# Performance work log

Measured on AMD Instinct MI355X. Metric: run time of the kernel, lower is better.

## Reference

```python
import jax, jax.numpy as jnp
import numpy as np

D, DFF, H = 768, 3072, 12
HD = D // H
EPS = 1e-12

def _ln(t, gamma, beta):
    mu = t.mean(-1, keepdims=True)
    var = jnp.mean((t - mu) ** 2, -1, keepdims=True)
    return gamma * (t - mu) / jnp.sqrt(var + EPS) + beta

def setup_inputs() -> dict:
    key = jax.random.key(0)
    ks = jax.random.split(key, 16)
    s = 0.02
    x = jax.random.normal(ks[0], (2, 2048, D), jnp.float32)
    mask = jnp.ones((2, 2048), jnp.float32)
    def lin(k, out_d, in_d):
        kw, kb = jax.random.split(k)
        return (jax.random.normal(kw, (out_d, in_d), jnp.float32) * s,
                jnp.zeros((out_d,), jnp.float32))
    Wq, bq = lin(ks[1], D, D)
    Wk, bk = lin(ks[2], D, D)
    Wv, bv = lin(ks[3], D, D)
    Wp, bp = lin(ks[4], D, D)
    W1, bf1 = lin(ks[5], DFF, D)
    W2, bf2 = lin(ks[6], D, DFF)
    g1 = jnp.ones((D,), jnp.float32); be1 = jnp.zeros((D,), jnp.float32)
    g2 = jnp.ones((D,), jnp.float32); be2 = jnp.zeros((D,), jnp.float32)
    return dict(x=x, mask=mask, Wq=Wq, bq=bq, Wk=Wk, bk=bk, Wv=Wv, bv=bv,
                Wp=Wp, bp=bp, g1=g1, be1=be1, W1=W1, bf1=bf1, W2=W2, bf2=bf2,
                g2=g2, be2=be2)

def reference(x, mask, Wq, bq, Wk, bk, Wv, bv, Wp, bp, g1, be1, W1, bf1, W2, bf2, g2, be2):
    B, S, _ = x.shape
    # projections (torch Linear: x @ W^T + b)
    q = (x @ Wq.T + bq).reshape(B, S, H, HD).transpose(0, 2, 1, 3)  # [B,H,S,HD]
    k = (x @ Wk.T + bk).reshape(B, S, H, HD).transpose(0, 2, 1, 3)
    v = (x @ Wv.T + bv).reshape(B, S, H, HD).transpose(0, 2, 1, 3)
    scores = jnp.einsum('bhqd,bhkd->bhqk', q, k) / jnp.sqrt(jnp.float32(HD))
    scores = scores - 10000.0 * (1.0 - mask[:, None, None, :])
    p = jax.nn.softmax(scores, axis=-1)  # dropout is identity at eval
    h = jnp.einsum('bhqk,bhkd->bqhd', p, v).reshape(B, S, D)
    h = h @ Wp.T + bp
    x1 = _ln(x + h, g1, be1)
    ff = jax.nn.gelu(x1 @ W1.T + bf1, approximate=False) @ W2.T + bf2
    return _ln(x1 + ff, g2, be2)
```

## Files before the change

kernel.cpp:

```cpp
#include <hip/hip_runtime.h>
#include <hip/hip_bf16.h>
#include <math.h>

#define D_MODEL 768
#define D_FF    3072
#define N_HEAD  12
#define HEAD_D  64
#define BATCH   2
#define SEQ     2048
#define QKV_LD  2304

typedef __attribute__((ext_vector_type(8))) short short8;
typedef __attribute__((ext_vector_type(8))) unsigned short ushort8;
typedef __attribute__((ext_vector_type(4))) float f32x4;

__device__ inline unsigned short f2bf(float f) {
    union { __hip_bfloat16 b; unsigned short u; } cv;
    cv.b = __float2bfloat16(f);
    return cv.u;
}

__device__ inline float bf2f(unsigned short u) {
    union { unsigned int i; float f; } cv;
    cv.i = ((unsigned int)u) << 16;
    return cv.f;
}

__device__ inline void async_load16(const void* g, void* l) {
    __builtin_amdgcn_global_load_lds(
        (const __attribute__((address_space(1))) void*)g,
        (__attribute__((address_space(3))) void*)l, 16, 0, 0);
}

__global__ __launch_bounds__(256) void conv_fused(
    const float* __restrict__ x,
    const float* __restrict__ Wq, const float* __restrict__ Wk,
    const float* __restrict__ Wv, const float* __restrict__ Wp,
    const float* __restrict__ W1, const float* __restrict__ W2,
    const float* __restrict__ bq, const float* __restrict__ bk,
    const float* __restrict__ bv,
    unsigned short* __restrict__ xb, unsigned short* __restrict__ wqkvb,
    unsigned short* __restrict__ wpb, unsigned short* __restrict__ w1b,
    unsigned short* __restrict__ w2b, float* __restrict__ bqkv)
{
    int bid = blockIdx.x;
    const float* src; unsigned short* dst; int base;
    if      (bid < 3072) { src = x;  dst = xb;              base = bid;        }
    else if (bid < 3648) { src = Wq; dst = wqkvb;           base = bid - 3072; }
    else if (bid < 4224) { src = Wk; dst = wqkvb + 589824;  base = bid - 3648; }
    else if (bid < 4800) { src = Wv; dst = wqkvb + 1179648; base = bid - 4224; }
    else if (bid < 5376) { src = Wp; dst = wpb;             base = bid - 4800; }
    else if (bid < 7680) { src = W1; dst = w1b;             base = bid - 5376; }
    else if (bid < 9984) { src = W2; dst = w2b;             base = bid - 7680; }
    else {
        for (int j = threadIdx.x; j < QKV_LD; j += 256)
            bqkv[j] = (j < 768) ? bq[j] : (j < 1536) ? bk[j - 768] : bv[j - 1536];
        return;
    }
    int i = (base * 256 + threadIdx.x) * 4;
    float4 v = *(const float4*)(src + i);
    ushort4 o4;
    o4.x = f2bf(v.x); o4.y = f2bf(v.y); o4.z = f2bf(v.z); o4.w = f2bf(v.w);
    *(ushort4*)(dst + i) = o4;
}

#define NSTAGE 3

__global__ __launch_bounds__(256) void gemm_bf16(
    const unsigned short* __restrict__ A, int lda,
    const unsigned short* __restrict__ W, int ldw,
    const float* __restrict__ bias,
    const unsigned short* __restrict__ resb, int ldr,
    float* __restrict__ outf, unsigned short* __restrict__ outb,
    float* __restrict__ pacc, int ldo,
    int M, int N, int K, int mode)
{
    __shared__ unsigned short As[NSTAGE][128 * 32];
    __shared__ unsigned short Bs[NSTAGE][128 * 32];

    const int t    = threadIdx.x;
    const int lane = t & 63;
    const int wv   = t >> 6;
    const int wm   = wv >> 1;
    const int wn   = wv & 1;
    const int bm   = blockIdx.y * 128;
    const int bn   = blockIdx.x * 128;
    const int kz   = blockIdx.z;
    const int Kc   = K / gridDim.z;

    const int qd   = lane >> 4;
    const int l16  = lane & 15;

    f32x4 acc[4][4];
    #pragma unroll
    for (int i = 0; i < 4; i++)
        #pragma unroll
        for (int j = 0; j < 4; j++)
            acc[i][j] = (f32x4){0.f, 0.f, 0.f, 0.f};

    const int srow = lane >> 2;
    const int sseg = (lane & 3) * 8;
    const int r0   = (wv * 2 + 0) * 16 + srow;
    const int r1   = (wv * 2 + 1) * 16 + srow;
    const size_t gA0 = (size_t)(bm + r0) * lda + sseg;
    const size_t gA1 = (size_t)(bm + r1) * lda + sseg;
    const size_t gB0 = (size_t)(bn + r0) * ldw + sseg;
    const size_t gB1 = (size_t)(bn + r1) * ldw + sseg;
    const int c0 = (wv * 2 + 0) * 512;
    const int c1 = (wv * 2 + 1) * 512;

    const int kbeg  = kz * Kc;
    const int niter = Kc / 32;

    async_load16(A + gA0 + kbeg, &As[0][c0]);
    async_load16(W + gB0 + kbeg, &Bs[0][c0]);
    async_load16(A + gA1 + kbeg, &As[0][c1]);
    async_load16(W + gB1 + kbeg, &Bs[0][c1]);
    if (niter > 1) {
        async_load16(A + gA0 + kbeg + 32, &As[1][c0]);
        async_load16(W + gB0 + kbeg + 32, &Bs[1][c0]);
        async_load16(A + gA1 + kbeg + 32, &As[1][c1]);
        async_load16(W + gB1 + kbeg + 32, &Bs[1][c1]);
    }
    if (niter > 2) {
        async_load16(A + gA0 + kbeg + 64, &As[2][c0]);
        async_load16(W + gB0 + kbeg + 64, &Bs[2][c0]);
        async_load16(A + gA1 + kbeg + 64, &As[2][c1]);
        async_load16(W + gB1 + kbeg + 64, &Bs[2][c1]);
    }

    int stage = 0;
    for (int it = 0; it < niter; it++) {
        const int rem = niter - 1 - it;
        if (rem >= 2)      __builtin_amdgcn_s_waitcnt(0x0F78);
        else if (rem == 1) __builtin_amdgcn_s_waitcnt(0x0F74);
        else               __builtin_amdgcn_s_waitcnt(0x0F70);
        __builtin_amdgcn_s_barrier();

        short8 af[4], bf[4];
        #pragma unroll
        for (int mt = 0; mt < 4; mt++)
            af[mt] = *(const short8*)(&As[stage][(wm * 64 + mt * 16 + l16) * 32 + qd * 8]);
        #pragma unroll
        for (int nt = 0; nt < 4; nt++)
            bf[nt] = *(const short8*)(&Bs[stage][(wn * 64 + nt * 16 + l16) * 32 + qd * 8]);
        #pragma unroll
        for (int mt = 0; mt < 4; mt++)
            #pragma unroll
            for (int nt = 0; nt < 4; nt++)
                acc[mt][nt] = __builtin_amdgcn_mfma_f32_16x16x32_bf16(
                    af[mt], bf[nt], acc[mt][nt], 0, 0, 0);

        __builtin_amdgcn_s_barrier();
        if (it + NSTAGE < niter) {
            const int kn = kbeg + (it + NSTAGE) * 32;
            async_load16(A + gA0 + kn, &As[stage][c0]);
            async_load16(W + gB0 + kn, &Bs[stage][c0]);
            async_load16(A + gA1 + kn, &As[stage][c1]);
            async_load16(W + gB1 + kn, &Bs[stage][c1]);
        }
        stage = (stage == NSTAGE - 1) ? 0 : stage + 1;
    }

    #pragma unroll
    for (int mt = 0; mt < 4; mt++) {
        #pragma unroll
        for (int nt = 0; nt < 4; nt++) {
            int col = bn + wn * 64 + nt * 16 + l16;
            float bv = (kz == 0) ? bias[col] : 0.f;
            #pragma unroll
            for (int r = 0; r < 4; r++) {
                int row = bm + wm * 64 + mt * 16 + qd * 4 + r;
                if (kz != 0) {
                    pacc[(size_t)row * ldo + col] = acc[mt][nt][r];
                    continue;
                }
                float v = acc[mt][nt][r] + bv;
                if (mode == 1) {
                    v += bf2f(resb[(size_t)row * ldr + col]);
                    outf[(size_t)row * ldo + col] = v;
                } else if (mode == 2) {
                    v = 0.5f * v * (1.0f + erff(v * 0.70710678118654752f));
                    outb[(size_t)row * ldo + col] = f2bf(v);
                } else if (mode == 3) {
                    outb[(size_t)row * ldo + col] = f2bf(v);
                } else {
                    outf[(size_t)row * ldo + col] = v;
                }
            }
        }
    }
}

#define ASTR 72

__global__ __launch_bounds__(256) void attn_mfma(
    const unsigned short* __restrict__ qkv, const float* __restrict__ mask,
    unsigned short* __restrict__ out)
{
    __shared__ __align__(16) unsigned short Ks[64 * ASTR];
    __shared__ __align__(16) unsigned short Vt[64 * ASTR];
    __shared__ float Ms[64];

    const int t    = threadIdx.x;
    const int lane = t & 63;
    const int wv   = t >> 6;
    const int l16  = lane & 15;
    const int quad = lane >> 4;
    const int q0   = blockIdx.x * 64;
    const int bh   = blockIdx.y;
    const int h    = bh % N_HEAD;
    const int b    = bh / N_HEAD;

    const unsigned short* qb = qkv + (size_t)b * SEQ * QKV_LD + h * HEAD_D;
    const unsigned short* kb = qb + 768;
    const unsigned short* vb = qb + 1536;

    const int srow = t >> 2;
    const int sc0  = (t & 3) * 16;
    const int sigrow = (srow & 0x23) | ((srow & 0x04) << 2) | ((srow & 0x18) >> 1);
    const int vslot  = srow ^ ((t & 3) << 3);

    {
        const ushort8* src = (const ushort8*)(qb + (size_t)(q0 + srow) * QKV_LD + sc0);
        *(ushort8*)&Ks[srow * ASTR + sc0]     = src[0];
        *(ushort8*)&Ks[srow * ASTR + sc0 + 8] = src[1];
    }
    __syncthreads();
    short8 bq0 = *(const short8*)&Ks[(wv * 16 + l16) * ASTR + quad * 8];
    short8 bq1 = *(const short8*)&Ks[(wv * 16 + l16) * ASTR + 32 + quad * 8];
    __syncthreads();

    f32x4 o[4];
    #pragma unroll
    for (int i = 0; i < 4; i++) o[i] = (f32x4){0.f, 0.f, 0.f, 0.f};
    float m_st = -INFINITY, l_st = 0.f;

    for (int kt = 0; kt < SEQ / 64; kt++) {
        const int key0 = kt * 64;
        {
            const ushort8* ksrc = (const ushort8*)(kb + (size_t)(key0 + srow) * QKV_LD + sc0);
            *(ushort8*)&Ks[sigrow * ASTR + sc0]     = ksrc[0];
            *(ushort8*)&Ks[sigrow * ASTR + sc0 + 8] = ksrc[1];
            const ushort8* vsrc = (const ushort8*)(vb + (size_t)(key0 + srow) * QKV_LD + sc0);
            ushort8 v0 = vsrc[0], v1 = vsrc[1];
            #pragma unroll
            for (int j = 0; j < 8; j++) Vt[(sc0 + j) * ASTR + vslot] = v0[j];
            #pragma unroll
            for (int j = 0; j < 8; j++) Vt[(sc0 + 8 + j) * ASTR + vslot] = v1[j];
            if (t < 64) Ms[t] = -10000.0f * (1.0f - mask[b * SEQ + key0 + t]);
        }
        __syncthreads();

        f32x4 st[4];
        #pragma unroll
        for (int bi = 0; bi < 4; bi++) {
            const int krow = (bi * 16 + l16) * ASTR;
            short8 k0 = *(const short8*)&Ks[krow + quad * 8];
            short8 k1 = *(const short8*)&Ks[krow + 32 + quad * 8];
            f32x4 z = (f32x4){0.f, 0.f, 0.f, 0.f};
            z = __builtin_amdgcn_mfma_f32_16x16x32_bf16(k0, bq0, z, 0, 0, 0);
            st[bi] = __builtin_amdgcn_mfma_f32_16x16x32_bf16(k1, bq1, z, 0, 0, 0);
        }

        float p[4][4];
        float mx = -3.0e38f;
        #pragma unroll
        for (int bi = 0; bi < 4; bi++) {
            #pragma unroll
            for (int r = 0; r < 4; r++) {
                float s = fmaf(st[bi][r], 0.125f,
                               Ms[((bi >> 1) << 5) + (quad << 3) + ((bi & 1) << 2) + r]);
                p[bi][r] = s;
                mx = fmaxf(mx, s);
            }
        }
        mx = fmaxf(mx, __shfl_xor(mx, 16, 64));
        mx = fmaxf(mx, __shfl_xor(mx, 32, 64));
        float m_new = fmaxf(m_st, mx);
        float alpha = __expf(m_st - m_new);
        m_st = m_new;
        float ls = 0.f;
        #pragma unroll
        for (int bi = 0; bi < 4; bi++) {
            #pragma unroll
            for (int r = 0; r < 4; r++) {
                p[bi][r] = __expf(p[bi][r] - m_new);
                ls += p[bi][r];
            }
        }
        ls += __shfl_xor(ls, 16, 64);
        ls += __shfl_xor(ls, 32, 64);
        l_st = l_st * alpha + ls;

        float ar[4];
        #pragma unroll
        for (int r = 0; r < 4; r++) ar[r] = __shfl(alpha, quad * 4 + r, 64);
        #pragma unroll
        for (int nt = 0; nt < 4; nt++)
            #pragma unroll
            for (int r = 0; r < 4; r++)
                o[nt][r] *= ar[r];

        short8 pf0, pf1;
        #pragma unroll
        for (int bsel = 0; bsel < 2; bsel++) {
            #pragma unroll
            for (int r = 0; r < 4; r++) {
                pf0[bsel * 4 + r] = (short)f2bf(p[bsel][r]);
                pf1[bsel * 4 + r] = (short)f2bf(p[2 + bsel][r]);
            }
        }

        #pragma unroll
        for (int nt = 0; nt < 4; nt++) {
            const int vrow = (nt * 16 + l16) * ASTR;
            short8 v0 = *(const short8*)&Vt[vrow + ((quad * 8) ^ (nt << 3))];
            short8 v1 = *(const short8*)&Vt[vrow + ((32 + quad * 8) ^ (nt << 3))];
            o[nt] = __builtin_amdgcn_mfma_f32_16x16x32_bf16(pf0, v0, o[nt], 0, 0, 0);
            o[nt] = __builtin_amdgcn_mfma_f32_16x16x32_bf16(pf1, v1, o[nt], 0, 0, 0);
        }
        __syncthreads();
    }

    float inv = 1.0f / l_st;
    float ir[4];
    #pragma unroll
    for (int r = 0; r < 4; r++) ir[r] = __shfl(inv, quad * 4 + r, 64);
    #pragma unroll
    for (int nt = 0; nt < 4; nt++) {
        #pragma unroll
        for (int r = 0; r < 4; r++) {
            int qi = q0 + wv * 16 + quad * 4 + r;
            out[(size_t)(b * SEQ + qi) * D_MODEL + h * HEAD_D + nt * 16 + l16] =
                f2bf(o[nt][r] * ir[r]);
        }
    }
}

__global__ __launch_bounds__(256) void ln_kernel(
    const float* __restrict__ in, const float* __restrict__ in2,
    const float* __restrict__ g, const float* __restrict__ be,
    float* __restrict__ outf, unsigned short* __restrict__ outb)
{
    const int row = blockIdx.x;
    const int t   = threadIdx.x;
    const float* rp  = in  + (size_t)row * D_MODEL;
    const float* rp2 = in2 ? in2 + (size_t)row * D_MODEL : nullptr;

    float vals[3];
    float s = 0.f, s2 = 0.f;
    #pragma unroll
    for (int i = 0; i < 3; i++) {
        float x = rp[t + i * 256];
        if (rp2) x += rp2[t + i * 256];
        vals[i] = x;
        s += x; s2 += x * x;
    }
    #pragma unroll
    for (int off = 32; off >= 1; off >>= 1) {
        s  += __shfl_xor(s,  off, 64);
        s2 += __shfl_xor(s2, off, 64);
    }
    __shared__ float rs[4], rs2[4];
    __shared__ float mu_s, rstd_s;
    const int wave = t >> 6, lane = t & 63;
    if (lane == 0) { rs[wave] = s; rs2[wave] = s2; }
    __syncthreads();
    if (t == 0) {
        float S1 = rs[0] + rs[1] + rs[2] + rs[3];
        float S2 = rs2[0] + rs2[1] + rs2[2] + rs2[3];
        float mu  = S1 * (1.0f / D_MODEL);
        float var = S2 * (1.0f / D_MODEL) - mu * mu;
        mu_s = mu;
        rstd_s = rsqrtf(var + 1e-12f);
    }
    __syncthreads();
    const float mu = mu_s, rstd = rstd_s;
    #pragma unroll
    for (int i = 0; i < 3; i++) {
        int c = t + i * 256;
        float o = g[c] * (vals[i] - mu) * rstd + be[c];
        if (outf) outf[(size_t)row * D_MODEL + c] = o;
        if (outb) outb[(size_t)row * D_MODEL + c] = f2bf(o);
    }
}

extern "C" void kernel_launch(void* const* d_in, const int* in_sizes, int n_in,
                              void* d_out, int out_size, void* d_ws, size_t ws_size,
                              hipStream_t stream)
{
    const float* x    = (const float*)d_in[0];
    const float* mask = (const float*)d_in[1];
    const float* Wq   = (const float*)d_in[2];
    const float* bq   = (const float*)d_in[3];
    const float* Wk   = (const float*)d_in[4];
    const float* bk   = (const float*)d_in[5];
    const float* Wv   = (const float*)d_in[6];
    const float* bv   = (const float*)d_in[7];
    const float* Wp   = (const float*)d_in[8];
    const float* bp   = (const float*)d_in[9];
    const float* g1   = (const float*)d_in[10];
    const float* be1  = (const float*)d_in[11];
    const float* W1   = (const float*)d_in[12];
    const float* bf1  = (const float*)d_in[13];
    const float* W2   = (const float*)d_in[14];
    const float* bf2  = (const float*)d_in[15];
    const float* g2   = (const float*)d_in[16];
    const float* be2  = (const float*)d_in[17];

    const int M = BATCH * SEQ;

    char* ws = (char*)d_ws;
    unsigned short* qkvb  = (unsigned short*)(ws + 0);
    unsigned short* ff1b  = (unsigned short*)(ws + 0);
    unsigned short* xb    = (unsigned short*)(ws + 25165824);
    unsigned short* hb    = (unsigned short*)(ws + 31457280);
    unsigned short* x1b   = (unsigned short*)(ws + 31457280);
    float*          y0    = (float*)(ws + 37748736);
    unsigned short* wqkvb = (unsigned short*)(ws + 50331648);
    unsigned short* wpb   = (unsigned short*)(ws + 53870592);
    unsigned short* w1b   = (unsigned short*)(ws + 55050240);
    unsigned short* w2b   = (unsigned short*)(ws + 59768832);
    float*          bqkv  = (float*)(ws + 64487424);
    float*          p1    = (float*)(ws + 64496640);

    dim3 blk(256);

    conv_fused<<<dim3(9985), blk, 0, stream>>>(
        x, Wq, Wk, Wv, Wp, W1, W2, bq, bk, bv,
        xb, wqkvb, wpb, w1b, w2b, bqkv);

    gemm_bf16<<<dim3(QKV_LD / 128, M / 128, 1), blk, 0, stream>>>(
        xb, D_MODEL, wqkvb, D_MODEL, bqkv, nullptr, 0,
        nullptr, qkvb, nullptr, QKV_LD, M, QKV_LD, D_MODEL, 3);

    attn_mfma<<<dim3(SEQ / 64, BATCH * N_HEAD), blk, 0, stream>>>(qkvb, mask, hb);

    gemm_bf16<<<dim3(D_MODEL / 128, M / 128, 2), blk, 0, stream>>>(
        hb, D_MODEL, wpb, D_MODEL, bp, xb, D_MODEL,
        y0, nullptr, p1, D_MODEL, M, D_MODEL, D_MODEL, 1);

    ln_kernel<<<dim3(M), blk, 0, stream>>>(y0, p1, g1, be1, nullptr, x1b);

    gemm_bf16<<<dim3(D_FF / 128, M / 128, 1), blk, 0, stream>>>(
        x1b, D_MODEL, w1b, D_MODEL, bf1, nullptr, 0,
        nullptr, ff1b, nullptr, D_FF, M, D_FF, D_MODEL, 2);

    gemm_bf16<<<dim3(D_MODEL / 128, M / 128, 2), blk, 0, stream>>>(
        ff1b, D_FF, w2b, D_FF, bf2, x1b, D_MODEL,
        y0, nullptr, p1, D_MODEL, M, D_MODEL, D_FF, 1);

    ln_kernel<<<dim3(M), blk, 0, stream>>>(y0, p1, g2, be2, (float*)d_out, nullptr);
}
```

Baseline: 371.0 us.

## Pre-transpose V in a separate kernel, register-prefetch attention tiles, restructure GEMM pipeline

A new vtrans kernel writes V transposed per head into the workspace. Attention can then store V tiles to LDS with vector writes instead of scalar scattered writes, and it prefetches the next K/V/mask tile into registers while computing the current one. The GEMM main loop is reworked to issue the load two stages ahead right after the barrier, which drops the second barrier per iteration, and the third initial prefetch is removed. The cost is an extra kernel launch, an extra round trip of V through global memory, and a possible risk of LDS stage reuse if NSTAGE is below 3.

```diff
diff --git a/kernel.cpp b/kernel.cpp
--- a/kernel.cpp
+++ b/kernel.cpp
@@ -122,20 +122,21 @@
         async_load16(A + gA1 + kbeg + 32, &As[1][c1]);
         async_load16(W + gB1 + kbeg + 32, &Bs[1][c1]);
     }
-    if (niter > 2) {
-        async_load16(A + gA0 + kbeg + 64, &As[2][c0]);
-        async_load16(W + gB0 + kbeg + 64, &Bs[2][c0]);
-        async_load16(A + gA1 + kbeg + 64, &As[2][c1]);
-        async_load16(W + gB1 + kbeg + 64, &Bs[2][c1]);
-    }
 
     int stage = 0;
     for (int it = 0; it < niter; it++) {
-        const int rem = niter - 1 - it;
-        if (rem >= 2)      __builtin_amdgcn_s_waitcnt(0x0F78);
-        else if (rem == 1) __builtin_amdgcn_s_waitcnt(0x0F74);
-        else               __builtin_amdgcn_s_waitcnt(0x0F70);
+        if (it + 1 < niter) __builtin_amdgcn_s_waitcnt(0x0F74);
+        else                __builtin_amdgcn_s_waitcnt(0x0F70);
         __builtin_amdgcn_s_barrier();
+
+        if (it + 2 < niter) {
+            const int sn = (stage + 2 >= NSTAGE) ? stage + 2 - NSTAGE : stage + 2;
+            const int kn = kbeg + (it + 2) * 32;
+            async_load16(A + gA0 + kn, &As[sn][c0]);
+            async_load16(W + gB0 + kn, &Bs[sn][c0]);
+            async_load16(A + gA1 + kn, &As[sn][c1]);
+            async_load16(W + gB1 + kn, &Bs[sn][c1]);
+        }
 
         short8 af[4], bf[4];
         #pragma unroll
@@ -151,14 +152,6 @@
                 acc[mt][nt] = __builtin_amdgcn_mfma_f32_16x16x32_bf16(
                     af[mt], bf[nt], acc[mt][nt], 0, 0, 0);
 
-        __builtin_amdgcn_s_barrier();
-        if (it + NSTAGE < niter) {
-            const int kn = kbeg + (it + NSTAGE) * 32;
-            async_load16(A + gA0 + kn, &As[stage][c0]);
-            async_load16(W + gB0 + kn, &Bs[stage][c0]);
-            async_load16(A + gA1 + kn, &As[stage][c1]);
-            async_load16(W + gB1 + kn, &Bs[stage][c1]);
-        }
         stage = (stage == NSTAGE - 1) ? 0 : stage + 1;
     }
 
@@ -192,11 +185,40 @@
     }
 }
 
+__global__ __launch_bounds__(256) void vtrans(
+    const unsigned short* __restrict__ qkv, unsigned short* __restrict__ vT)
+{
+    __shared__ unsigned short T[64 * 72];
+    const int t   = threadIdx.x;
+    const int kt  = blockIdx.x;
+    const int bh  = blockIdx.y;
+    const int h   = bh % N_HEAD;
+    const int b   = bh / N_HEAD;
+    const int row = t >> 2;
+    const int c0  = (t & 3) * 16;
+
+    const unsigned short* src =
+        qkv + (size_t)(b * SEQ + kt * 64 + row) * QKV_LD + 1536 + h * HEAD_D + c0;
+    *(ushort8*)&T[row * 72 + c0]     = *(const ushort8*)src;
+    *(ushort8*)&T[row * 72 + c0 + 8] = *(const ushort8*)(src + 8);
+    __syncthreads();
+
+    const int d = t >> 2;
+    ushort8 o0, o1;
+    #pragma unroll
+    for (int j = 0; j < 8; j++) o0[j] = T[(c0 + j) * 72 + d];
+    #pragma unroll
+    for (int j = 0; j < 8; j++) o1[j] = T[(c0 + 8 + j) * 72 + d];
+    unsigned short* dst = vT + ((size_t)bh * HEAD_D + d) * SEQ + kt * 64 + c0;
+    *(ushort8*)dst       = o0;
+    *(ushort8*)(dst + 8) = o1;
+}
+
 #define ASTR 72
 
 __global__ __launch_bounds__(256) void attn_mfma(
-    const unsigned short* __restrict__ qkv, const float* __restrict__ mask,
-    unsigned short* __restrict__ out)
+    const unsigned short* __restrict__ qkv, const unsigned short* __restrict__ vT,
+    const float* __restrict__ mask, unsigned short* __restrict__ out)
 {
     __shared__ __align__(16) unsigned short Ks[64 * ASTR];
     __shared__ __align__(16) unsigned short Vt[64 * ASTR];
@@ -212,14 +234,13 @@
     const int h    = bh % N_HEAD;
     const int b    = bh / N_HEAD;
 
-    const unsigned short* qb = qkv + (size_t)b * SEQ * QKV_LD + h * HEAD_D;
-    const unsigned short* kb = qb + 768;
-    const unsigned short* vb = qb + 1536;
+    const unsigned short* qb  = qkv + (size_t)b * SEQ * QKV_LD + h * HEAD_D;
+    const unsigned short* kb  = qb + 768;
+    const unsigned short* vtb = vT + (size_t)bh * HEAD_D * SEQ;
 
     const int srow = t >> 2;
     const int sc0  = (t & 3) * 16;
     const int sigrow = (srow & 0x23) | ((srow & 0x04) << 2) | ((srow & 0x18) >> 1);
-    const int vslot  = srow ^ ((t & 3) << 3);
 
     {
         const ushort8* src = (const ushort8*)(qb + (size_t)(q0 + srow) * QKV_LD + sc0);
@@ -236,21 +257,32 @@
     for (int i = 0; i < 4; i++) o[i] = (f32x4){0.f, 0.f, 0.f, 0.f};
     float m_st = -INFINITY, l_st = 0.f;
 
+    ushort8 rk0, rk1, rv0, rv1;
+    float rm = 1.0f;
+    {
+        const ushort8* ksrc = (const ushort8*)(kb + (size_t)srow * QKV_LD + sc0);
+        rk0 = ksrc[0]; rk1 = ksrc[1];
+        const ushort8* vsrc = (const ushort8*)(vtb + (size_t)srow * SEQ + sc0);
+        rv0 = vsrc[0]; rv1 = vsrc[1];
+        if (t < 64) rm = mask[b * SEQ + t];
+    }
+
     for (int kt = 0; kt < SEQ / 64; kt++) {
-        const int key0 = kt * 64;
-        {
-            const ushort8* ksrc = (const ushort8*)(kb + (size_t)(key0 + srow) * QKV_LD + sc0);
-            *(ushort8*)&Ks[sigrow * ASTR + sc0]     = ksrc[0];
-            *(ushort8*)&Ks[sigrow * ASTR + sc0 + 8] = ksrc[1];
-            const ushort8* vsrc = (const ushort8*)(vb + (size_t)(key0 + srow) * QKV_LD + sc0);
-            ushort8 v0 = vsrc[0], v1 = vsrc[1];
-            #pragma unroll
-            for (int j = 0; j < 8; j++) Vt[(sc0 + j) * ASTR + vslot] = v0[j];
-            #pragma unroll
-            for (int j = 0; j < 8; j++) Vt[(sc0 + 8 + j) * ASTR + vslot] = v1[j];
-            if (t < 64) Ms[t] = -10000.0f * (1.0f - mask[b * SEQ + key0 + t]);
-        }
+        *(ushort8*)&Ks[sigrow * ASTR + sc0]     = rk0;
+        *(ushort8*)&Ks[sigrow * ASTR + sc0 + 8] = rk1;
+        *(ushort8*)&Vt[srow * ASTR + sc0]       = rv0;
+        *(ushort8*)&Vt[srow * ASTR + sc0 + 8]   = rv1;
+        if (t < 64) Ms[t] = -10000.0f * (1.0f - rm);
         __syncthreads();
+
+        if (kt + 1 < SEQ / 64) {
+            const int kn = (kt + 1) * 64;
+            const ushort8* ksrc = (const ushort8*)(kb + (size_t)(kn + srow) * QKV_LD + sc0);
+            rk0 = ksrc[0]; rk1 = ksrc[1];
+            const ushort8* vsrc = (const ushort8*)(vtb + (size_t)srow * SEQ + kn + sc0);
+            rv0 = vsrc[0]; rv1 = vsrc[1];
+            if (t < 64) rm = mask[b * SEQ + kn + t];
+        }
 
         f32x4 st[4];
         #pragma unroll
@@ -315,8 +347,8 @@
         #pragma unroll
         for (int nt = 0; nt < 4; nt++) {
             const int vrow = (nt * 16 + l16) * ASTR;
-            short8 v0 = *(const short8*)&Vt[vrow + ((quad * 8) ^ (nt << 3))];
-            short8 v1 = *(const short8*)&Vt[vrow + ((32 + quad * 8) ^ (nt << 3))];
+            short8 v0 = *(const short8*)&Vt[vrow + quad * 8];
+            short8 v1 = *(const short8*)&Vt[vrow + 32 + quad * 8];
             o[nt] = __builtin_amdgcn_mfma_f32_16x16x32_bf16(pf0, v0, o[nt], 0, 0, 0);
             o[nt] = __builtin_amdgcn_mfma_f32_16x16x32_bf16(pf1, v1, o[nt], 0, 0, 0);
         }
@@ -424,6 +456,7 @@
     unsigned short* w2b   = (unsigned short*)(ws + 59768832);
     float*          bqkv  = (float*)(ws + 64487424);
     float*          p1    = (float*)(ws + 64496640);
+    unsigned short* vTb   = (unsigned short*)(ws + 77079552);
 
     dim3 blk(256);
 
@@ -435,7 +468,9 @@
         xb, D_MODEL, wqkvb, D_MODEL, bqkv, nullptr, 0,
         nullptr, qkvb, nullptr, QKV_LD, M, QKV_LD, D_MODEL, 3);
 
-    attn_mfma<<<dim3(SEQ / 64, BATCH * N_HEAD), blk, 0, stream>>>(qkvb, mask, hb);
+    vtrans<<<dim3(SEQ / 64, BATCH * N_HEAD), blk, 0, stream>>>(qkvb, vTb);
+
+    attn_mfma<<<dim3(SEQ / 64, BATCH * N_HEAD), blk, 0, stream>>>(qkvb, vTb, mask, hb);
 
     gemm_bf16<<<dim3(D_MODEL / 128, M / 128, 2), blk, 0, stream>>>(
         hb, D_MODEL, wpb, D_MODEL, bp, xb, D_MODEL,
```

Measured after the change: 367.3 us. About the same (-1.0%).
